# Kernel tuning notes

Measured on AMD Instinct MI355X. Metric: run time of the kernel, lower is better.

Reference implementation:

```python
import jax, jax.numpy as jnp
import numpy as np

N = 50000      # nodes
E = 800000     # edges (avg degree 16)
IN = 128       # in_channels
OUT = 64       # out_channels
HID = 2 * OUT  # 128, hidden width of conv1
EPS = 1e-5     # BatchNorm eps


def _edge_norm(edge_index):
    # PyG ChebConv with sym normalization, lambda_max=2: L_hat = -D^{-1/2} A D^{-1/2}
    src, dst = edge_index[0], edge_index[1]
    deg = jax.ops.segment_sum(jnp.ones((E,), jnp.float32), src, num_segments=N)
    dinv = jnp.where(deg > 0, jax.lax.rsqrt(jnp.maximum(deg, 1.0)), 0.0)
    return -dinv[src] * dinv[dst]


def _cheb(x, src, dst, norm, W0, W1, b):
    # K=2 Chebyshev conv: Tx0 = x, Tx1 = L_hat x (sparse propagate)
    tx1 = jax.ops.segment_sum(x[src] * norm[:, None], dst, num_segments=N)
    return x @ W0 + tx1 @ W1 + b


def setup_inputs() -> dict:
    key = jax.random.key(0)
    ks = jax.random.split(key, 14)
    g = lambda k, shp, fan: jax.random.normal(k, shp, jnp.float32) / np.sqrt(fan)
    return {
        "x": jax.random.normal(ks[0], (N, IN), jnp.float32),
        "edge_index": jax.random.randint(ks[1], (2, E), 0, N, dtype=jnp.int32),
        "W1_0": g(ks[2], (IN, HID), IN),
        "W1_1": g(ks[3], (IN, HID), IN),
        "b1": jnp.zeros((HID,), jnp.float32),
        "gamma": jnp.ones((HID,), jnp.float32),
        "beta": jnp.zeros((HID,), jnp.float32),
        "Wmu_0": g(ks[4], (HID, OUT), HID),
        "Wmu_1": g(ks[5], (HID, OUT), HID),
        "b_mu": jnp.zeros((OUT,), jnp.float32),
        "Wls_0": g(ks[6], (HID, OUT), HID),
        "Wls_1": g(ks[7], (HID, OUT), HID),
        "b_ls": jnp.zeros((OUT,), jnp.float32),
    }


def reference(x, edge_index, W1_0, W1_1, b1, gamma, beta,
              Wmu_0, Wmu_1, b_mu, Wls_0, Wls_1, b_ls):
    src, dst = edge_index[0], edge_index[1]
    norm = _edge_norm(edge_index)
    h = _cheb(x, src, dst, norm, W1_0, W1_1, b1)         # [N, HID]
    # BatchNorm1d (training mode: batch statistics over nodes)
    mean = jnp.mean(h, axis=0)
    var = jnp.var(h, axis=0)
    h = (h - mean) * jax.lax.rsqrt(var + EPS) * gamma + beta
    h = jax.nn.relu(h)
    mu = _cheb(h, src, dst, norm, Wmu_0, Wmu_1, b_mu)    # [N, OUT]
    logstd = _cheb(h, src, dst, norm, Wls_0, Wls_1, b_ls)
    return (mu, logstd)
```

## Files before the change

### kernel.cpp

```cpp
#include <hip/hip_runtime.h>
#include <cstddef>
#include <cstdint>

static constexpr int IN_C  = 128;
static constexpr float BN_EPS = 1e-5f;
static constexpr int OUT_C = 64;

static constexpr int CS_C = 32;
static constexpr int CS_R = 8;
static constexpr int CS_RANGE = 6250;

using bf16x8 = __attribute__((ext_vector_type(8))) short;
using f32x4  = __attribute__((ext_vector_type(4))) float;

__device__ __forceinline__ ushort f2bf(float f) {
    uint u = __float_as_uint(f);
    u += 0x7fffu + ((u >> 16) & 1u);
    return (ushort)(u >> 16);
}
__device__ __forceinline__ uint pack2(float a, float b) {
    return (uint)f2bf(a) | ((uint)f2bf(b) << 16);
}
__device__ __forceinline__ float bf_lo(uint v) { return __uint_as_float(v << 16); }
__device__ __forceinline__ float bf_hi(uint v) { return __uint_as_float(v & 0xffff0000u); }

__device__ __forceinline__ int swz8(int row, int g) { return (g ^ ((row >> 1) & 3)) * 8; }

__global__ __launch_bounds__(1024) void hist_conv_k(
    const int* __restrict__ src, const int* __restrict__ dst,
    ushort* __restrict__ hsrc_part, ushort* __restrict__ hdst_part,
    int N, int E, int chunk, int range, int nb_hist, int nb_x,
    const float* __restrict__ x, ushort* __restrict__ xb,
    const float* __restrict__ W1_0, const float* __restrict__ W1_1,
    const float* __restrict__ b1,
    const float* __restrict__ Wmu_0, const float* __restrict__ Wmu_1,
    const float* __restrict__ b_mu,
    const float* __restrict__ Wls_0, const float* __restrict__ Wls_1,
    const float* __restrict__ b_ls,
    ushort* __restrict__ Wt1, ushort* __restrict__ Wt2,
    float* __restrict__ bias1, float* __restrict__ bias2) {
    __shared__ int hs_[CS_RANGE];
    __shared__ int hd_[CS_RANGE];
    int bid = blockIdx.x;
    if (bid < nb_hist) {
        int c = bid & (CS_C - 1);
        int r = bid / CS_C;
        int base = r * range;
        int hi = min(base + range, N);
        int rsz = hi - base;
        for (int j = threadIdx.x; j < rsz; j += 1024) { hs_[j] = 0; hd_[j] = 0; }
        __syncthreads();
        int e0 = c * chunk, e1 = min(e0 + chunk, E);
        for (int i = e0 + threadIdx.x; i < e1; i += 1024) {
            int s = src[i];
            if (s >= base && s < hi) atomicAdd(&hs_[s - base], 1);
            int t = dst[i];
            if (t >= base && t < hi) atomicAdd(&hd_[t - base], 1);
        }
        __syncthreads();
        for (int j = threadIdx.x; j < rsz; j += 1024) {
            hsrc_part[(size_t)c * N + base + j] = (ushort)hs_[j];
            hdst_part[(size_t)c * N + base + j] = (ushort)hd_[j];
        }
    } else if (bid < nb_hist + nb_x) {
        int i = (bid - nb_hist) * 1024 + threadIdx.x;
        if (i < N * 64) {
            float2 v = ((const float2*)x)[i];
            ((uint*)xb)[i] = pack2(v.x, v.y);
        }
    } else {
        int idx = (bid - nb_hist - nb_x) * 1024 + threadIdx.x;
        int which = idx >> 15;
        int c = (idx >> 8) & 127;
        int k = idx & 255;
        if (which == 0) {
            float v = (k < 128) ? W1_0[k * 128 + c] : W1_1[(k - 128) * 128 + c];
            Wt1[c * 256 + k] = f2bf(v);
            if (k == 0) bias1[c] = b1[c];
        } else {
            float v;
            if (c < 64) v = (k < 128) ? Wmu_0[k * 64 + c] : Wmu_1[(k - 128) * 64 + c];
            else        v = (k < 128) ? Wls_0[k * 64 + (c - 64)] : Wls_1[(k - 128) * 64 + (c - 64)];
            Wt2[c * 256 + k] = f2bf(v);
            if (k == 0) bias2[c] = (c < 64) ? b_mu[c] : b_ls[c - 64];
        }
    }
}

__global__ __launch_bounds__(256) void count_k(
    const ushort* __restrict__ hsrc_part, const ushort* __restrict__ hdst_part,
    float* __restrict__ dinv, int* __restrict__ cnt_dst,
    int* __restrict__ bsum, float* __restrict__ stats, int N) {
    __shared__ int sw[4];
    int tid = threadIdx.x;
    if (blockIdx.x == 0) stats[tid] = 0.f;
    int v = blockIdx.x * 256 + tid;
    int b = 0;
    if (v < N) {
        int a = 0;
        for (int c = 0; c < CS_C; ++c) {
            a += hsrc_part[(size_t)c * N + v];
            b += hdst_part[(size_t)c * N + v];
        }
        dinv[v] = (a > 0) ? rsqrtf((float)a) : 0.f;
        cnt_dst[v] = b;
    }
    int t = b;
    #pragma unroll
    for (int off = 1; off < 64; off <<= 1) t += __shfl_xor(t, off, 64);
    if ((tid & 63) == 0) sw[tid >> 6] = t;
    __syncthreads();
    if (tid == 0) bsum[blockIdx.x] = sw[0] + sw[1] + sw[2] + sw[3];
}

__global__ __launch_bounds__(256) void phase3_k(
    const int* __restrict__ cnt, const int* __restrict__ bsum,
    int* __restrict__ row_ptr, const ushort* __restrict__ hdst_part,
    int* __restrict__ offs, int n, int nb) {
    __shared__ int sbp[4];
    __shared__ int swv[4];
    int tid = threadIdx.x;
    int lane = tid & 63, wave = tid >> 6;
    int bv = (tid < nb && tid < (int)blockIdx.x) ? bsum[tid] : 0;
    int t = bv;
    #pragma unroll
    for (int off = 1; off < 64; off <<= 1) t += __shfl_xor(t, off, 64);
    if (lane == 0) sbp[wave] = t;
    int v = blockIdx.x * 256 + tid;
    int c = (v < n) ? cnt[v] : 0;
    int s = c;
    #pragma unroll
    for (int off = 1; off < 64; off <<= 1) {
        int u = __shfl_up(s, off, 64);
        if (lane >= off) s += u;
    }
    if (lane == 63) swv[wave] = s;
    __syncthreads();
    int bpre = sbp[0] + sbp[1] + sbp[2] + sbp[3];
    int wexcl = 0;
    for (int w = 0; w < wave; ++w) wexcl += swv[w];
    int st = bpre + wexcl + (s - c);
    if (v < n) row_ptr[v + 1] = st + c;
    if (v == 0) row_ptr[0] = 0;
    int r = st;
    for (int ch = 0; ch < CS_C; ++ch) {
        size_t idx = (size_t)ch * n + v;
        if (v < n) {
            offs[idx] = r;
            r += hdst_part[idx];
        }
    }
}

__global__ __launch_bounds__(1024) void scatter_k(
    const int* __restrict__ src, const int* __restrict__ dst,
    const int* __restrict__ off, int* __restrict__ col,
    int N, int E, int chunk, int range) {
    __shared__ int cur[CS_RANGE];
    int c = blockIdx.x & (CS_C - 1);
    int r = blockIdx.x / CS_C;
    int base = r * range;
    int hi = min(base + range, N);
    int rsz = hi - base;
    for (int j = threadIdx.x; j < rsz; j += 1024)
        cur[j] = off[(size_t)c * N + base + j];
    __syncthreads();
    int e0 = c * chunk, e1 = min(e0 + chunk, E);
    for (int i = e0 + threadIdx.x; i < e1; i += 1024) {
        int t = dst[i];
        if (t >= base && t < hi) {
            int pos = atomicAdd(&cur[t - base], 1);
            col[pos] = src[i];
        }
    }
}

#define FMA8(V, D)                                                            \
  { float v0_ = bf_lo((V).x), v1_ = bf_hi((V).x), v2_ = bf_lo((V).y),         \
          v3_ = bf_hi((V).y), v4_ = bf_lo((V).z), v5_ = bf_hi((V).z),         \
          v6_ = bf_lo((V).w), v7_ = bf_hi((V).w);                             \
    if (BN) {                                                                 \
      v0_ = fmaxf(v0_ * sc[0] + sh[0], 0.f);                                  \
      v1_ = fmaxf(v1_ * sc[1] + sh[1], 0.f);                                  \
      v2_ = fmaxf(v2_ * sc[2] + sh[2], 0.f);                                  \
      v3_ = fmaxf(v3_ * sc[3] + sh[3], 0.f);                                  \
      v4_ = fmaxf(v4_ * sc[4] + sh[4], 0.f);                                  \
      v5_ = fmaxf(v5_ * sc[5] + sh[5], 0.f);                                  \
      v6_ = fmaxf(v6_ * sc[6] + sh[6], 0.f);                                  \
      v7_ = fmaxf(v7_ * sc[7] + sh[7], 0.f);                                  \
    }                                                                         \
    acc[0] += v0_ * (D); acc[1] += v1_ * (D); acc[2] += v2_ * (D);            \
    acc[3] += v3_ * (D); acc[4] += v4_ * (D); acc[5] += v5_ * (D);            \
    acc[6] += v6_ * (D); acc[7] += v7_ * (D); }

template <int BN>
__global__ __launch_bounds__(256) void propagate4_k(
    const uint4* __restrict__ xs, uint4* __restrict__ out,
    const int* __restrict__ row_ptr, const int* __restrict__ col,
    const float* __restrict__ dinv, int n,
    const float* __restrict__ stats, const float* __restrict__ gamma,
    const float* __restrict__ beta, float inv_n) {
    int wid = (blockIdx.x * 256 + threadIdx.x) >> 6;
    if (wid >= n) return;
    int lane = threadIdx.x & 63;
    int g = lane >> 4, li = lane & 15;
    float sc[8], sh[8];
    if (BN) {
        #pragma unroll
        for (int j = 0; j < 8; ++j) {
            int f = li * 8 + j;
            float mean = stats[f] * inv_n;
            float var = stats[128 + f] * inv_n - mean * mean;
            float s = gamma[f] * rsqrtf(var + BN_EPS);
            sc[j] = s;
            sh[j] = beta[f] - mean * s;
        }
    }
    int s = row_ptr[wid], e = row_ptr[wid + 1];
    float acc[8];
    #pragma unroll
    for (int k = 0; k < 8; ++k) acc[k] = 0.f;
    int i = s + g;
    for (; i + 12 < e; i += 16) {
        int c0 = col[i];
        int c1 = col[i + 4];
        int c2 = col[i + 8];
        int c3 = col[i + 12];
        float d0 = dinv[c0], d1 = dinv[c1], d2 = dinv[c2], d3 = dinv[c3];
        uint4 v0 = xs[(size_t)c0 * 16 + li];
        uint4 v1 = xs[(size_t)c1 * 16 + li];
        uint4 v2 = xs[(size_t)c2 * 16 + li];
        uint4 v3 = xs[(size_t)c3 * 16 + li];
        FMA8(v0, d0); FMA8(v1, d1); FMA8(v2, d2); FMA8(v3, d3);
    }
    for (; i < e; i += 4) {
        int c0 = col[i];
        float d0 = dinv[c0];
        uint4 v0 = xs[(size_t)c0 * 16 + li];
        FMA8(v0, d0);
    }
    #pragma unroll
    for (int k = 0; k < 8; ++k) {
        acc[k] += __shfl_xor(acc[k], 16, 64);
        acc[k] += __shfl_xor(acc[k], 32, 64);
    }
    if (g == 0) {
        float scl = -dinv[wid];
        uint4 o;
        o.x = pack2(acc[0] * scl, acc[1] * scl);
        o.y = pack2(acc[2] * scl, acc[3] * scl);
        o.z = pack2(acc[4] * scl, acc[5] * scl);
        o.w = pack2(acc[6] * scl, acc[7] * scl);
        out[(size_t)wid * 16 + li] = o;
    }
}

template <int MODE>
__global__ __launch_bounds__(256) void gemm_mfma_k(
    const ushort* __restrict__ A0, const ushort* __restrict__ A1,
    const ushort* __restrict__ Wt, const float* __restrict__ bias,
    ushort* __restrict__ Cb, float* __restrict__ Cmu, float* __restrict__ Cls,
    float* __restrict__ stats, int n,
    const float* __restrict__ gamma, const float* __restrict__ beta,
    float inv_n) {
    __shared__ ushort sA[64][32];
    __shared__ ushort sW[128][32];
    __shared__ float smS[4][128];
    __shared__ float smQ[4][128];
    __shared__ float sp[256];

    int tid = threadIdx.x;
    int block_row = blockIdx.x * 64;
    int wave = tid >> 6, lane = tid & 63;
    int col_base = lane & 15;
    int quad = lane >> 4;
    int m_local = wave * 16 + col_base;

    if (MODE == 1) {
        if (tid < 128) {
            float mean = stats[tid] * inv_n;
            float var = stats[128 + tid] * inv_n - mean * mean;
            float s = gamma[tid] * rsqrtf(var + BN_EPS);
            sp[tid] = s;
            sp[128 + tid] = beta[tid] - mean * s;
        }
        __syncthreads();
    }

    f32x4 acc[8];
    #pragma unroll
    for (int t = 0; t < 8; ++t) acc[t] = (f32x4){0.f, 0.f, 0.f, 0.f};

    for (int k0 = 0; k0 < 256; k0 += 32) {
        {
            int row = tid >> 2, g = tid & 3;
            int grow = block_row + row;
            int kc = k0 + g * 8;
            uint4 v = make_uint4(0, 0, 0, 0);
            if (grow < n) {
                const ushort* srcp = (kc < 128) ? (A0 + (size_t)grow * 128 + kc)
                                                : (A1 + (size_t)grow * 128 + (kc - 128));
                v = *(const uint4*)srcp;
                if (MODE == 1 && kc < 128) {
                    float a0 = fmaxf(bf_lo(v.x) * sp[kc + 0] + sp[128 + kc + 0], 0.f);
                    float a1 = fmaxf(bf_hi(v.x) * sp[kc + 1] + sp[128 + kc + 1], 0.f);
                    float a2 = fmaxf(bf_lo(v.y) * sp[kc + 2] + sp[128 + kc + 2], 0.f);
                    float a3 = fmaxf(bf_hi(v.y) * sp[kc + 3] + sp[128 + kc + 3], 0.f);
                    float a4 = fmaxf(bf_lo(v.z) * sp[kc + 4] + sp[128 + kc + 4], 0.f);
                    float a5 = fmaxf(bf_hi(v.z) * sp[kc + 5] + sp[128 + kc + 5], 0.f);
                    float a6 = fmaxf(bf_lo(v.w) * sp[kc + 6] + sp[128 + kc + 6], 0.f);
                    float a7 = fmaxf(bf_hi(v.w) * sp[kc + 7] + sp[128 + kc + 7], 0.f);
                    v.x = pack2(a0, a1); v.y = pack2(a2, a3);
                    v.z = pack2(a4, a5); v.w = pack2(a6, a7);
                }
            }
            *(uint4*)&sA[row][swz8(row, g)] = v;
        }
        #pragma unroll
        for (int i = tid; i < 512; i += 256) {
            int c = i >> 2, g = i & 3;
            *(uint4*)&sW[c][swz8(c, g)] = *(const uint4*)(Wt + (size_t)c * 256 + k0 + g * 8);
        }
        __syncthreads();
        bf16x8 af = *(const bf16x8*)&sA[m_local][swz8(m_local, quad)];
        #pragma unroll
        for (int t = 0; t < 8; ++t) {
            int wr = t * 16 + col_base;
            bf16x8 bfr = *(const bf16x8*)&sW[wr][swz8(wr, quad)];
            acc[t] = __builtin_amdgcn_mfma_f32_16x16x32_bf16(af, bfr, acc[t], 0, 0, 0);
        }
        __syncthreads();
    }

    int row_l = wave * 16 + quad * 4;
    #pragma unroll
    for (int t = 0; t < 8; ++t) {
        int col = t * 16 + col_base;
        float b = bias[col];
        float s = 0.f, q = 0.f;
        #pragma unroll
        for (int r = 0; r < 4; ++r) {
            int grow = block_row + row_l + r;
            if (grow < n) {
                float v = acc[t][r] + b;
                if (MODE == 0) {
                    Cb[(size_t)grow * 128 + col] = f2bf(v);
                    s += v; q += v * v;
                } else {
                    if (col < 64) Cmu[(size_t)grow * 64 + col] = v;
                    else          Cls[(size_t)grow * 64 + (col - 64)] = v;
                }
            }
        }
        if (MODE == 0) {
            s += __shfl_xor(s, 16, 64); s += __shfl_xor(s, 32, 64);
            q += __shfl_xor(q, 16, 64); q += __shfl_xor(q, 32, 64);
            if (quad == 0) { smS[wave][col] = s; smQ[wave][col] = q; }
        }
    }
    if (MODE == 0) {
        __syncthreads();
        if (tid < 128) {
            float s = smS[0][tid] + smS[1][tid] + smS[2][tid] + smS[3][tid];
            float q = smQ[0][tid] + smQ[1][tid] + smQ[2][tid] + smQ[3][tid];
            atomicAdd(&stats[tid], s);
            atomicAdd(&stats[128 + tid], q);
        }
    }
}

extern "C" void kernel_launch(void* const* d_in, const int* in_sizes, int n_in,
                              void* d_out, int out_size, void* d_ws, size_t ws_size,
                              hipStream_t stream) {
    const float* x = (const float*)d_in[0];
    const int* edge_index = (const int*)d_in[1];
    const float* W1_0 = (const float*)d_in[2];
    const float* W1_1 = (const float*)d_in[3];
    const float* b1 = (const float*)d_in[4];
    const float* gamma = (const float*)d_in[5];
    const float* beta = (const float*)d_in[6];
    const float* Wmu_0 = (const float*)d_in[7];
    const float* Wmu_1 = (const float*)d_in[8];
    const float* b_mu = (const float*)d_in[9];
    const float* Wls_0 = (const float*)d_in[10];
    const float* Wls_1 = (const float*)d_in[11];
    const float* b_ls = (const float*)d_in[12];

    const int N = in_sizes[0] / IN_C;
    const int E = in_sizes[1] / 2;
    const int* src = edge_index;
    const int* dst = edge_index + E;

    char* w = (char*)d_ws;
    auto alloc = [&](size_t bytes) {
        char* p = w;
        w += (bytes + 15) & ~(size_t)15;
        return p;
    };
    float* stats = (float*)alloc(256 * 4);
    int* row_ptr = (int*)alloc((size_t)(N + 1) * 4);
    int* bsum    = (int*)alloc(256 * 4);
    float* dinv  = (float*)alloc((size_t)N * 4);
    int* cnt_dst = (int*)alloc((size_t)N * 4);
    int* col     = (int*)alloc((size_t)E * 4);
    ushort* hsrc_part = (ushort*)alloc((size_t)CS_C * N * 2);
    ushort* hdst_part = (ushort*)alloc((size_t)CS_C * N * 2);
    int* offs    = (int*)alloc((size_t)CS_C * N * 4);
    ushort* x_bf  = (ushort*)alloc((size_t)N * 128 * 2);
    ushort* xp_bf = (ushort*)alloc((size_t)N * 128 * 2);
    ushort* h_bf  = (ushort*)alloc((size_t)N * 128 * 2);
    ushort* Wt1   = (ushort*)alloc(128 * 256 * 2);
    ushort* Wt2   = (ushort*)alloc(128 * 256 * 2);
    float* bias1  = (float*)alloc(128 * 4);
    float* bias2  = (float*)alloc(128 * 4);

    float* out_mu = (float*)d_out;
    float* out_ls = out_mu + (size_t)N * OUT_C;

    int chunk = (E + CS_C - 1) / CS_C;
    int range = (N + CS_R - 1) / CS_R;
    int NBLK = (N + 255) / 256;
    int nb_hist = CS_R * CS_C;
    int nb_x = (N * 64 + 1023) / 1024;
    int nb_w = 64;
    float inv_n = 1.f / (float)N;

    hist_conv_k<<<nb_hist + nb_x + nb_w, 1024, 0, stream>>>(
        src, dst, hsrc_part, hdst_part, N, E, chunk, range, nb_hist, nb_x,
        x, x_bf, W1_0, W1_1, b1, Wmu_0, Wmu_1, b_mu, Wls_0, Wls_1, b_ls,
        Wt1, Wt2, bias1, bias2);
    count_k<<<NBLK, 256, 0, stream>>>(hsrc_part, hdst_part, dinv, cnt_dst, bsum, stats, N);
    phase3_k<<<NBLK, 256, 0, stream>>>(cnt_dst, bsum, row_ptr, hdst_part, offs, N, NBLK);
    scatter_k<<<nb_hist, 1024, 0, stream>>>(src, dst, offs, col, N, E, chunk, range);

    int pb = (N + 3) / 4;
    propagate4_k<0><<<pb, 256, 0, stream>>>((const uint4*)x_bf, (uint4*)xp_bf,
                                            row_ptr, col, dinv, N,
                                            nullptr, nullptr, nullptr, 0.f);

    int gb = (N + 63) / 64;
    gemm_mfma_k<0><<<gb, 256, 0, stream>>>(x_bf, xp_bf, Wt1, bias1, h_bf,
                                           nullptr, nullptr, stats, N,
                                           nullptr, nullptr, 0.f);

    propagate4_k<1><<<pb, 256, 0, stream>>>((const uint4*)h_bf, (uint4*)xp_bf,
                                            row_ptr, col, dinv, N,
                                            stats, gamma, beta, inv_n);

    gemm_mfma_k<1><<<gb, 256, 0, stream>>>(h_bf, xp_bf, Wt2, bias2, nullptr,
                                           out_mu, out_ls, stats, N,
                                           gamma, beta, inv_n);
}
```

Before: 279.4 us.

## Split propagate across feature chunks and store CSR column indices as 16-bit

The sparse propagate kernel is restructured so each wave handles one node and one 32-feature quarter. A wave now processes 16 edges at once, with 4 lanes per edge, in place of 4 edges with 16 lanes each. The block index is remapped so the four feature chunks of a node group launch next to each other, which should help L2 reuse of the gathered rows. CSR column indices are now stored as ushort, which halves index traffic but only works while N fits in 16 bits. The change also drops the 4-way unrolled independent loads and issues 4x more waves, and short-degree nodes leave more lanes idle per iteration.

```diff
diff --git a/kernel.cpp b/kernel.cpp
--- a/kernel.cpp
+++ b/kernel.cpp
@@ -154,7 +154,7 @@
 
 __global__ __launch_bounds__(1024) void scatter_k(
     const int* __restrict__ src, const int* __restrict__ dst,
-    const int* __restrict__ off, int* __restrict__ col,
+    const int* __restrict__ off, ushort* __restrict__ col,
     int N, int E, int chunk, int range) {
     __shared__ int cur[CS_RANGE];
     int c = blockIdx.x & (CS_C - 1);
@@ -170,88 +170,89 @@
         int t = dst[i];
         if (t >= base && t < hi) {
             int pos = atomicAdd(&cur[t - base], 1);
-            col[pos] = src[i];
-        }
-    }
-}
-
-#define FMA8(V, D)                                                            \
-  { float v0_ = bf_lo((V).x), v1_ = bf_hi((V).x), v2_ = bf_lo((V).y),         \
-          v3_ = bf_hi((V).y), v4_ = bf_lo((V).z), v5_ = bf_hi((V).z),         \
-          v6_ = bf_lo((V).w), v7_ = bf_hi((V).w);                             \
-    if (BN) {                                                                 \
-      v0_ = fmaxf(v0_ * sc[0] + sh[0], 0.f);                                  \
-      v1_ = fmaxf(v1_ * sc[1] + sh[1], 0.f);                                  \
-      v2_ = fmaxf(v2_ * sc[2] + sh[2], 0.f);                                  \
-      v3_ = fmaxf(v3_ * sc[3] + sh[3], 0.f);                                  \
-      v4_ = fmaxf(v4_ * sc[4] + sh[4], 0.f);                                  \
-      v5_ = fmaxf(v5_ * sc[5] + sh[5], 0.f);                                  \
-      v6_ = fmaxf(v6_ * sc[6] + sh[6], 0.f);                                  \
-      v7_ = fmaxf(v7_ * sc[7] + sh[7], 0.f);                                  \
-    }                                                                         \
-    acc[0] += v0_ * (D); acc[1] += v1_ * (D); acc[2] += v2_ * (D);            \
-    acc[3] += v3_ * (D); acc[4] += v4_ * (D); acc[5] += v5_ * (D);            \
-    acc[6] += v6_ * (D); acc[7] += v7_ * (D); }
+            col[pos] = (ushort)src[i];
+        }
+    }
+}
 
 template <int BN>
-__global__ __launch_bounds__(256) void propagate4_k(
+__global__ __launch_bounds__(256) void propagate_fs_k(
     const uint4* __restrict__ xs, uint4* __restrict__ out,
-    const int* __restrict__ row_ptr, const int* __restrict__ col,
+    const int* __restrict__ row_ptr, const ushort* __restrict__ colu,
     const float* __restrict__ dinv, int n,
     const float* __restrict__ stats, const float* __restrict__ gamma,
     const float* __restrict__ beta, float inv_n) {
-    int wid = (blockIdx.x * 256 + threadIdx.x) >> 6;
-    if (wid >= n) return;
+    int bid = blockIdx.x;
+    int r8 = bid & 7;
+    int c = r8 & 3;
+    int ng = (bid >> 3) * 2 + (r8 >> 2);
+    int wave = threadIdx.x >> 6;
+    int node = ng * 4 + wave;
+    if (node >= n) return;
     int lane = threadIdx.x & 63;
-    int g = lane >> 4, li = lane & 15;
+    int slot = lane >> 2;
+    int fl = lane & 3;
+
     float sc[8], sh[8];
     if (BN) {
+        int f0 = c * 32 + fl * 8;
         #pragma unroll
         for (int j = 0; j < 8; ++j) {
-            int f = li * 8 + j;
+            int f = f0 + j;
             float mean = stats[f] * inv_n;
             float var = stats[128 + f] * inv_n - mean * mean;
-            float s = gamma[f] * rsqrtf(var + BN_EPS);
-            sc[j] = s;
-            sh[j] = beta[f] - mean * s;
-        }
-    }
-    int s = row_ptr[wid], e = row_ptr[wid + 1];
+            float s_ = gamma[f] * rsqrtf(var + BN_EPS);
+            sc[j] = s_;
+            sh[j] = beta[f] - mean * s_;
+        }
+    }
+
+    int s = row_ptr[node], e = row_ptr[node + 1];
+    int deg = e - s;
     float acc[8];
     #pragma unroll
     for (int k = 0; k < 8; ++k) acc[k] = 0.f;
-    int i = s + g;
-    for (; i + 12 < e; i += 16) {
-        int c0 = col[i];
-        int c1 = col[i + 4];
-        int c2 = col[i + 8];
-        int c3 = col[i + 12];
-        float d0 = dinv[c0], d1 = dinv[c1], d2 = dinv[c2], d3 = dinv[c3];
-        uint4 v0 = xs[(size_t)c0 * 16 + li];
-        uint4 v1 = xs[(size_t)c1 * 16 + li];
-        uint4 v2 = xs[(size_t)c2 * 16 + li];
-        uint4 v3 = xs[(size_t)c3 * 16 + li];
-        FMA8(v0, d0); FMA8(v1, d1); FMA8(v2, d2); FMA8(v3, d3);
-    }
-    for (; i < e; i += 4) {
-        int c0 = col[i];
-        float d0 = dinv[c0];
-        uint4 v0 = xs[(size_t)c0 * 16 + li];
-        FMA8(v0, d0);
-    }
+
+    int nt = (deg + 15) >> 4;
+    int em1 = e - 1;
+    int fidx = c * 4 + fl;
+    for (int t = 0; t < nt; ++t) {
+        int i = s + t * 16 + slot;
+        int j = min(i, em1);
+        int cj = (int)colu[j];
+        float d = (i < e) ? dinv[cj] : 0.f;
+        uint4 v = xs[(size_t)cj * 16 + fidx];
+        float p0 = bf_lo(v.x), p1 = bf_hi(v.x), p2 = bf_lo(v.y), p3 = bf_hi(v.y);
+        float p4 = bf_lo(v.z), p5 = bf_hi(v.z), p6 = bf_lo(v.w), p7 = bf_hi(v.w);
+        if (BN) {
+            p0 = fmaxf(p0 * sc[0] + sh[0], 0.f);
+            p1 = fmaxf(p1 * sc[1] + sh[1], 0.f);
+            p2 = fmaxf(p2 * sc[2] + sh[2], 0.f);
+            p3 = fmaxf(p3 * sc[3] + sh[3], 0.f);
+            p4 = fmaxf(p4 * sc[4] + sh[4], 0.f);
+            p5 = fmaxf(p5 * sc[5] + sh[5], 0.f);
+            p6 = fmaxf(p6 * sc[6] + sh[6], 0.f);
+            p7 = fmaxf(p7 * sc[7] + sh[7], 0.f);
+        }
+        acc[0] += p0 * d; acc[1] += p1 * d; acc[2] += p2 * d; acc[3] += p3 * d;
+        acc[4] += p4 * d; acc[5] += p5 * d; acc[6] += p6 * d; acc[7] += p7 * d;
+    }
+
     #pragma unroll
     for (int k = 0; k < 8; ++k) {
+        acc[k] += __shfl_xor(acc[k], 4, 64);
+        acc[k] += __shfl_xor(acc[k], 8, 64);
         acc[k] += __shfl_xor(acc[k], 16, 64);
         acc[k] += __shfl_xor(acc[k], 32, 64);
     }
-    if (g == 0) {
-        float scl = -dinv[wid];
+    if (slot == 0) {
+        float scl = -dinv[node];
         uint4 o;
         o.x = pack2(acc[0] * scl, acc[1] * scl);
         o.y = pack2(acc[2] * scl, acc[3] * scl);
         o.z = pack2(acc[4] * scl, acc[5] * scl);
         o.w = pack2(acc[6] * scl, acc[7] * scl);
-        out[(size_t)wid * 16 + li] = o;
+        out[(size_t)node * 16 + fidx] = o;
     }
 }
 
@@ -402,7 +403,7 @@
     int* bsum    = (int*)alloc(256 * 4);
     float* dinv  = (float*)alloc((size_t)N * 4);
     int* cnt_dst = (int*)alloc((size_t)N * 4);
-    int* col     = (int*)alloc((size_t)E * 4);
+    ushort* col  = (ushort*)alloc((size_t)E * 2);
     ushort* hsrc_part = (ushort*)alloc((size_t)CS_C * N * 2);
     ushort* hdst_part = (ushort*)alloc((size_t)CS_C * N * 2);
     int* offs    = (int*)alloc((size_t)CS_C * N * 4);
@@ -433,19 +434,20 @@
     phase3_k<<<NBLK, 256, 0, stream>>>(cnt_dst, bsum, row_ptr, hdst_part, offs, N, NBLK);
     scatter_k<<<nb_hist, 1024, 0, stream>>>(src, dst, offs, col, N, E, chunk, range);
 
-    int pb = (N + 3) / 4;
-    propagate4_k<0><<<pb, 256, 0, stream>>>((const uint4*)x_bf, (uint4*)xp_bf,
-                                            row_ptr, col, dinv, N,
-                                            nullptr, nullptr, nullptr, 0.f);
+    int ngroups = (N + 3) / 4;
+    int pb = 8 * ((ngroups + 1) / 2);
+    propagate_fs_k<0><<<pb, 256, 0, stream>>>((const uint4*)x_bf, (uint4*)xp_bf,
+                                              row_ptr, col, dinv, N,
+                                              nullptr, nullptr, nullptr, 0.f);
 
     int gb = (N + 63) / 64;
     gemm_mfma_k<0><<<gb, 256, 0, stream>>>(x_bf, xp_bf, Wt1, bias1, h_bf,
                                            nullptr, nullptr, stats, N,
                                            nullptr, nullptr, 0.f);
 
-    propagate4_k<1><<<pb, 256, 0, stream>>>((const uint4*)h_bf, (uint4*)xp_bf,
-                                            row_ptr, col, dinv, N,
-                                            stats, gamma, beta, inv_n);
+    propagate_fs_k<1><<<pb, 256, 0, stream>>>((const uint4*)h_bf, (uint4*)xp_bf,
+                                              row_ptr, col, dinv, N,
+                                              stats, gamma, beta, inv_n);
 
     gemm_mfma_k<1><<<gb, 256, 0, stream>>>(h_bf, xp_bf, Wt2, bias2, nullptr,
                                            out_mu, out_ls, stats, N,
```

Result: slower. 399.1 us (+42.8%).

## Use packed 16-bit shared histograms and ushort column indices for CSR build

Applied to the files above, without the earlier changes.

Histogram and scatter kernels now cover the full node range per edge chunk using two 16-bit counters packed per shared-memory word. This removes the 8-way range partitioning that re-read every edge chunk. Column indices are stored as 16-bit values, halving CSR index traffic in both propagation passes. The cost is fewer blocks (lower parallelism), a hard-coded node limit, and correctness only while node ids and per-chunk counts fit in 16 bits.

```diff
diff --git a/kernel.cpp b/kernel.cpp
--- a/kernel.cpp
+++ b/kernel.cpp
@@ -7,8 +7,8 @@
 static constexpr int OUT_C = 64;
 
 static constexpr int CS_C = 32;
-static constexpr int CS_R = 8;
-static constexpr int CS_RANGE = 6250;
+static constexpr int NMAX = 50000;
+static constexpr int NHALF = NMAX / 2;
 
 using bf16x8 = __attribute__((ext_vector_type(8))) short;
 using f32x4  = __attribute__((ext_vector_type(4))) float;
@@ -29,7 +29,7 @@
 __global__ __launch_bounds__(1024) void hist_conv_k(
     const int* __restrict__ src, const int* __restrict__ dst,
     ushort* __restrict__ hsrc_part, ushort* __restrict__ hdst_part,
-    int N, int E, int chunk, int range, int nb_hist, int nb_x,
+    int N, int E, int chunk, int nb_x,
     const float* __restrict__ x, ushort* __restrict__ xb,
     const float* __restrict__ W1_0, const float* __restrict__ W1_1,
     const float* __restrict__ b1,
@@ -39,37 +39,32 @@
     const float* __restrict__ b_ls,
     ushort* __restrict__ Wt1, ushort* __restrict__ Wt2,
     float* __restrict__ bias1, float* __restrict__ bias2) {
-    __shared__ int hs_[CS_RANGE];
-    __shared__ int hd_[CS_RANGE];
+    __shared__ uint hp[NHALF];
     int bid = blockIdx.x;
-    if (bid < nb_hist) {
-        int c = bid & (CS_C - 1);
-        int r = bid / CS_C;
-        int base = r * range;
-        int hi = min(base + range, N);
-        int rsz = hi - base;
-        for (int j = threadIdx.x; j < rsz; j += 1024) { hs_[j] = 0; hd_[j] = 0; }
+    int tid = threadIdx.x;
+    if (bid < 2 * CS_C) {
+        bool is_dst = (bid >= CS_C);
+        int c = is_dst ? bid - CS_C : bid;
+        const int* ea = is_dst ? dst : src;
+        ushort* outp = is_dst ? hdst_part : hsrc_part;
+        for (int j = tid; j < NHALF; j += 1024) hp[j] = 0u;
         __syncthreads();
         int e0 = c * chunk, e1 = min(e0 + chunk, E);
-        for (int i = e0 + threadIdx.x; i < e1; i += 1024) {
-            int s = src[i];
-            if (s >= base && s < hi) atomicAdd(&hs_[s - base], 1);
-            int t = dst[i];
-            if (t >= base && t < hi) atomicAdd(&hd_[t - base], 1);
-        }
-        __syncthreads();
-        for (int j = threadIdx.x; j < rsz; j += 1024) {
-            hsrc_part[(size_t)c * N + base + j] = (ushort)hs_[j];
-            hdst_part[(size_t)c * N + base + j] = (ushort)hd_[j];
-        }
-    } else if (bid < nb_hist + nb_x) {
-        int i = (bid - nb_hist) * 1024 + threadIdx.x;
+        for (int i = e0 + tid; i < e1; i += 1024) {
+            int s = ea[i];
+            atomicAdd(&hp[s >> 1], 1u << ((s & 1) * 16));
+        }
+        __syncthreads();
+        uint* op = (uint*)(outp + (size_t)c * N);
+        for (int j = tid; j < N / 2; j += 1024) op[j] = hp[j];
+    } else if (bid < 2 * CS_C + nb_x) {
+        int i = (bid - 2 * CS_C) * 1024 + tid;
         if (i < N * 64) {
             float2 v = ((const float2*)x)[i];
             ((uint*)xb)[i] = pack2(v.x, v.y);
         }
     } else {
-        int idx = (bid - nb_hist - nb_x) * 1024 + threadIdx.x;
+        int idx = (bid - 2 * CS_C - nb_x) * 1024 + tid;
         int which = idx >> 15;
         int c = (idx >> 8) & 127;
         int k = idx & 255;
@@ -154,24 +149,22 @@
 
 __global__ __launch_bounds__(1024) void scatter_k(
     const int* __restrict__ src, const int* __restrict__ dst,
-    const int* __restrict__ off, int* __restrict__ col,
-    int N, int E, int chunk, int range) {
-    __shared__ int cur[CS_RANGE];
-    int c = blockIdx.x & (CS_C - 1);
-    int r = blockIdx.x / CS_C;
-    int base = r * range;
-    int hi = min(base + range, N);
-    int rsz = hi - base;
-    for (int j = threadIdx.x; j < rsz; j += 1024)
-        cur[j] = off[(size_t)c * N + base + j];
+    const int* __restrict__ offs, ushort* __restrict__ col,
+    int N, int E, int chunk) {
+    __shared__ uint dp[NHALF];
+    int tid = threadIdx.x;
+    int c = blockIdx.x;
+    for (int j = tid; j < NHALF; j += 1024) dp[j] = 0u;
     __syncthreads();
+    const int* offc = offs + (size_t)c * N;
     int e0 = c * chunk, e1 = min(e0 + chunk, E);
-    for (int i = e0 + threadIdx.x; i < e1; i += 1024) {
+    for (int i = e0 + tid; i < e1; i += 1024) {
         int t = dst[i];
-        if (t >= base && t < hi) {
-            int pos = atomicAdd(&cur[t - base], 1);
-            col[pos] = src[i];
-        }
+        int s = src[i];
+        uint d = atomicAdd(&dp[t >> 1], 1u << ((t & 1) * 16));
+        uint delta = (d >> ((t & 1) * 16)) & 0xffffu;
+        int pos = offc[t] + (int)delta;
+        col[pos] = (ushort)s;
     }
 }
 
@@ -196,7 +189,7 @@
 template <int BN>
 __global__ __launch_bounds__(256) void propagate4_k(
     const uint4* __restrict__ xs, uint4* __restrict__ out,
-    const int* __restrict__ row_ptr, const int* __restrict__ col,
+    const int* __restrict__ row_ptr, const ushort* __restrict__ colu,
     const float* __restrict__ dinv, int n,
     const float* __restrict__ stats, const float* __restrict__ gamma,
     const float* __restrict__ beta, float inv_n) {
@@ -222,10 +215,10 @@
     for (int k = 0; k < 8; ++k) acc[k] = 0.f;
     int i = s + g;
     for (; i + 12 < e; i += 16) {
-        int c0 = col[i];
-        int c1 = col[i + 4];
-        int c2 = col[i + 8];
-        int c3 = col[i + 12];
+        int c0 = (int)colu[i];
+        int c1 = (int)colu[i + 4];
+        int c2 = (int)colu[i + 8];
+        int c3 = (int)colu[i + 12];
         float d0 = dinv[c0], d1 = dinv[c1], d2 = dinv[c2], d3 = dinv[c3];
         uint4 v0 = xs[(size_t)c0 * 16 + li];
         uint4 v1 = xs[(size_t)c1 * 16 + li];
@@ -234,7 +227,7 @@
         FMA8(v0, d0); FMA8(v1, d1); FMA8(v2, d2); FMA8(v3, d3);
     }
     for (; i < e; i += 4) {
-        int c0 = col[i];
+        int c0 = (int)colu[i];
         float d0 = dinv[c0];
         uint4 v0 = xs[(size_t)c0 * 16 + li];
         FMA8(v0, d0);
@@ -402,7 +395,7 @@
     int* bsum    = (int*)alloc(256 * 4);
     float* dinv  = (float*)alloc((size_t)N * 4);
     int* cnt_dst = (int*)alloc((size_t)N * 4);
-    int* col     = (int*)alloc((size_t)E * 4);
+    ushort* col  = (ushort*)alloc((size_t)E * 2);
     ushort* hsrc_part = (ushort*)alloc((size_t)CS_C * N * 2);
     ushort* hdst_part = (ushort*)alloc((size_t)CS_C * N * 2);
     int* offs    = (int*)alloc((size_t)CS_C * N * 4);
@@ -418,20 +411,18 @@
     float* out_ls = out_mu + (size_t)N * OUT_C;
 
     int chunk = (E + CS_C - 1) / CS_C;
-    int range = (N + CS_R - 1) / CS_R;
     int NBLK = (N + 255) / 256;
-    int nb_hist = CS_R * CS_C;
     int nb_x = (N * 64 + 1023) / 1024;
     int nb_w = 64;
     float inv_n = 1.f / (float)N;
 
-    hist_conv_k<<<nb_hist + nb_x + nb_w, 1024, 0, stream>>>(
-        src, dst, hsrc_part, hdst_part, N, E, chunk, range, nb_hist, nb_x,
+    hist_conv_k<<<2 * CS_C + nb_x + nb_w, 1024, 0, stream>>>(
+        src, dst, hsrc_part, hdst_part, N, E, chunk, nb_x,
         x, x_bf, W1_0, W1_1, b1, Wmu_0, Wmu_1, b_mu, Wls_0, Wls_1, b_ls,
         Wt1, Wt2, bias1, bias2);
     count_k<<<NBLK, 256, 0, stream>>>(hsrc_part, hdst_part, dinv, cnt_dst, bsum, stats, N);
     phase3_k<<<NBLK, 256, 0, stream>>>(cnt_dst, bsum, row_ptr, hdst_part, offs, N, NBLK);
-    scatter_k<<<nb_hist, 1024, 0, stream>>>(src, dst, offs, col, N, E, chunk, range);
+    scatter_k<<<CS_C, 1024, 0, stream>>>(src, dst, offs, col, N, E, chunk);
 
     int pb = (N + 3) / 4;
     propagate4_k<0><<<pb, 256, 0, stream>>>((const uint4*)x_bf, (uint4*)xp_bf,
```

After: 304.0 us. 1.09x slower.
